# Optimization experiments

Hardware: AMD Instinct MI355X
Metric: run time of the kernel (lower is better)

## Reference

```python
import jax, jax.numpy as jnp
import numpy as np

N_POINTS = 65536
DIM = 8
E0 = N_POINTS - 1      # H0 generators (edges killing components)
E1 = 2_000_000         # H1 generators (birth edge + death edge)


def setup_inputs() -> dict:
    key = jax.random.key(0)
    k1, k2, k3 = jax.random.split(key, 3)
    points = jax.random.normal(k1, (N_POINTS, DIM), dtype=jnp.float32)
    verts0 = jax.random.randint(k2, (E0, 2), 0, N_POINTS, dtype=jnp.int64)
    verts1 = jax.random.randint(k3, (E1, 4), 0, N_POINTS, dtype=jnp.int64)
    return {"points": points, "verts0": verts0, "verts1": verts1}


def reference(points, verts0, verts1):
    # H0 death times: distance between the two vertices of each killing edge.
    # deaths[i] = || points[verts0[i,0]] - points[verts0[i,1]] ||
    d0 = points[verts0[:, 0]] - points[verts0[:, 1]]        # [E0, D]
    deaths = jnp.linalg.norm(d0, axis=-1)                    # [E0]

    # H1 diagram: birth = ||p[v0]-p[v1]||, death = ||p[v2]-p[v3]||,
    # computed as paired gathers on columns (0,2) vs (1,3) like the original.
    a = points[verts1[:, jnp.array([0, 2])]]                 # [E1, 2, D]
    b = points[verts1[:, jnp.array([1, 3])]]                 # [E1, 2, D]
    dgm1 = jnp.linalg.norm(a - b, axis=-1)                   # [E1, 2]
    return deaths, dgm1
```

## Files before the change

kernel.cpp:

```cpp
#include <hip/hip_runtime.h>
#include <hip/hip_fp16.h>
#include <math.h>


typedef int  v2i __attribute__((ext_vector_type(2)));

__global__ __launch_bounds__(256) void cvt_kernel(
    const float* __restrict__ pts, __half* __restrict__ out, int n4) {
    int i = blockIdx.x * blockDim.x + threadIdx.x;
    if (i < n4) {
        float4 f = ((const float4*)pts)[i];
        __half2 h0 = __floats2half2_rn(f.x, f.y);
        __half2 h1 = __floats2half2_rn(f.z, f.w);
        ((__half2*)out)[2 * i]     = h0;
        ((__half2*)out)[2 * i + 1] = h1;
    }
}

__device__ __forceinline__ float2 u2f2(unsigned u) {
    __half2 h = *reinterpret_cast<__half2*>(&u);
    return __half22float2(h);
}

__device__ __forceinline__ float dist8h(const uint4* __restrict__ p, int ia, int ib) {
    uint4 a = p[ia];
    uint4 b = p[ib];
    float2 ax = u2f2(a.x), ay = u2f2(a.y), az = u2f2(a.z), aw = u2f2(a.w);
    float2 bx = u2f2(b.x), by = u2f2(b.y), bz = u2f2(b.z), bw = u2f2(b.w);
    float d0 = ax.x - bx.x, d1 = ax.y - bx.y;
    float d2 = ay.x - by.x, d3 = ay.y - by.y;
    float d4 = az.x - bz.x, d5 = az.y - bz.y;
    float d6 = aw.x - bw.x, d7 = aw.y - bw.y;
    float s = d0 * d0 + d1 * d1 + d2 * d2 + d3 * d3
            + d4 * d4 + d5 * d5 + d6 * d6 + d7 * d7;
    return sqrtf(s);
}

__global__ __launch_bounds__(256) void rips_kernel_h2(
    const __half* __restrict__ points16,
    const int* __restrict__ verts0,
    const int* __restrict__ verts1,
    float* __restrict__ out,
    int e0, int e1) {
    int tid = blockIdx.x * blockDim.x + threadIdx.x;
    const uint4* p = (const uint4*)points16;
    int n1 = 2 * e1;
    if (tid < n1) {
        v2i v = __builtin_nontemporal_load((const v2i*)verts1 + tid);
        float r = dist8h(p, v.x, v.y);
        __builtin_nontemporal_store(r, out + e0 + tid);
    } else {
        int j = tid - n1;
        if (j < e0) {
            v2i v = __builtin_nontemporal_load((const v2i*)verts0 + j);
            float r = dist8h(p, v.x, v.y);
            __builtin_nontemporal_store(r, out + j);
        }
    }
}

__device__ __forceinline__ float dist8f(const float4* __restrict__ p, int ia, int ib) {
    float4 a0 = p[2 * ia], a1 = p[2 * ia + 1];
    float4 b0 = p[2 * ib], b1 = p[2 * ib + 1];
    float d0 = a0.x - b0.x, d1 = a0.y - b0.y, d2 = a0.z - b0.z, d3 = a0.w - b0.w;
    float d4 = a1.x - b1.x, d5 = a1.y - b1.y, d6 = a1.z - b1.z, d7 = a1.w - b1.w;
    return sqrtf(d0*d0 + d1*d1 + d2*d2 + d3*d3 + d4*d4 + d5*d5 + d6*d6 + d7*d7);
}

__global__ __launch_bounds__(256) void rips_kernel_f2(
    const float* __restrict__ points,
    const int* __restrict__ verts0,
    const int* __restrict__ verts1,
    float* __restrict__ out,
    int e0, int e1) {
    int tid = blockIdx.x * blockDim.x + threadIdx.x;
    const float4* p = (const float4*)points;
    int n1 = 2 * e1;
    if (tid < n1) {
        v2i v = __builtin_nontemporal_load((const v2i*)verts1 + tid);
        float r = dist8f(p, v.x, v.y);
        __builtin_nontemporal_store(r, out + e0 + tid);
    } else {
        int j = tid - n1;
        if (j < e0) {
            v2i v = __builtin_nontemporal_load((const v2i*)verts0 + j);
            float r = dist8f(p, v.x, v.y);
            __builtin_nontemporal_store(r, out + j);
        }
    }
}

extern "C" void kernel_launch(void* const* d_in, const int* in_sizes, int n_in,
                              void* d_out, int out_size, void* d_ws, size_t ws_size,
                              hipStream_t stream) {
    const float* points = (const float*)d_in[0];
    const int* verts0   = (const int*)d_in[1];
    const int* verts1   = (const int*)d_in[2];
    float* out = (float*)d_out;

    int npts_flat = in_sizes[0];
    int e0 = in_sizes[1] / 2;
    int e1 = in_sizes[2] / 4;

    int total = 2 * e1 + e0;
    int block = 256;
    int grid = (total + block - 1) / block;

    size_t fp16_bytes = (size_t)npts_flat * sizeof(__half);
    if (ws_size >= fp16_bytes) {
        __half* p16 = (__half*)d_ws;
        int n4 = npts_flat / 4;
        cvt_kernel<<<(n4 + 255) / 256, 256, 0, stream>>>(points, p16, n4);
        rips_kernel_h2<<<grid, block, 0, stream>>>(p16, verts0, verts1, out, e0, e1);
    } else {
        rips_kernel_f2<<<grid, block, 0, stream>>>(points, verts0, verts1, out, e0, e1);
    }
}
```

Baseline: 120.3 us.

## Process two H1 rows per thread and swizzle blocks across XCDs

Each thread now handles two H1 rows, issuing two 16-byte index loads, eight independent fp16 point gathers and four output stores. The H0 edges and an odd-row tail get a separate path. Block indices are remapped so that contiguous ranges of work land on the same XCD, which should improve L2 locality. The aim is more memory-level parallelism per thread and fewer threads, at the cost of higher register pressure and one quarter as many waves available to hide latency.

```diff
diff --git a/kernel.cpp b/kernel.cpp
--- a/kernel.cpp
+++ b/kernel.cpp
@@ -3,7 +3,8 @@
 #include <math.h>
 
 
-typedef int  v2i __attribute__((ext_vector_type(2)));
+typedef int v4i __attribute__((ext_vector_type(4)));
+typedef int v2i __attribute__((ext_vector_type(2)));
 
 __global__ __launch_bounds__(256) void cvt_kernel(
     const float* __restrict__ pts, __half* __restrict__ out, int n4) {
@@ -22,9 +23,7 @@
     return __half22float2(h);
 }
 
-__device__ __forceinline__ float dist8h(const uint4* __restrict__ p, int ia, int ib) {
-    uint4 a = p[ia];
-    uint4 b = p[ib];
+__device__ __forceinline__ float dist8v(uint4 a, uint4 b) {
     float2 ax = u2f2(a.x), ay = u2f2(a.y), az = u2f2(a.z), aw = u2f2(a.w);
     float2 bx = u2f2(b.x), by = u2f2(b.y), bz = u2f2(b.z), bw = u2f2(b.w);
     float d0 = ax.x - bx.x, d1 = ax.y - bx.y;
@@ -36,25 +35,62 @@
     return sqrtf(s);
 }
 
-__global__ __launch_bounds__(256) void rips_kernel_h2(
+__device__ __forceinline__ int xcd_swizzle(int b, int nwg) {
+    int q = nwg >> 3, r = nwg & 7;
+    int xcd = b & 7, off = b >> 3;
+    int base = (xcd < r) ? xcd * (q + 1) : r * (q + 1) + (xcd - r) * q;
+    return base + off;
+}
+
+__global__ __launch_bounds__(256) void rips_kernel_h8(
     const __half* __restrict__ points16,
     const int* __restrict__ verts0,
     const int* __restrict__ verts1,
     float* __restrict__ out,
     int e0, int e1) {
-    int tid = blockIdx.x * blockDim.x + threadIdx.x;
+    int sb = xcd_swizzle(blockIdx.x, gridDim.x);
+    int tid = sb * blockDim.x + threadIdx.x;
     const uint4* p = (const uint4*)points16;
-    int n1 = 2 * e1;
-    if (tid < n1) {
-        v2i v = __builtin_nontemporal_load((const v2i*)verts1 + tid);
-        float r = dist8h(p, v.x, v.y);
-        __builtin_nontemporal_store(r, out + e0 + tid);
+    int npair = e1 >> 1;
+    int rem   = e1 & 1;
+    if (tid < npair) {
+        const v4i* v1 = (const v4i*)verts1;
+        v4i va = __builtin_nontemporal_load(v1 + 2 * tid);
+        v4i vb = __builtin_nontemporal_load(v1 + 2 * tid + 1);
+        uint4 g0 = p[va.x];
+        uint4 g1 = p[va.y];
+        uint4 g2 = p[va.z];
+        uint4 g3 = p[va.w];
+        uint4 g4 = p[vb.x];
+        uint4 g5 = p[vb.y];
+        uint4 g6 = p[vb.z];
+        uint4 g7 = p[vb.w];
+        float r0 = dist8v(g0, g1);
+        float r1 = dist8v(g2, g3);
+        float r2 = dist8v(g4, g5);
+        float r3 = dist8v(g6, g7);
+        float* o = out + e0 + 4 * tid;
+        __builtin_nontemporal_store(r0, o);
+        __builtin_nontemporal_store(r1, o + 1);
+        __builtin_nontemporal_store(r2, o + 2);
+        __builtin_nontemporal_store(r3, o + 3);
     } else {
-        int j = tid - n1;
-        if (j < e0) {
-            v2i v = __builtin_nontemporal_load((const v2i*)verts0 + j);
-            float r = dist8h(p, v.x, v.y);
-            __builtin_nontemporal_store(r, out + j);
+        int j = tid - npair;
+        if (j < rem) {
+            int row = e1 - 1;
+            v2i v = __builtin_nontemporal_load((const v2i*)verts1 + 2 * row);
+            v2i w = __builtin_nontemporal_load((const v2i*)verts1 + 2 * row + 1);
+            float r0 = dist8v(p[v.x], p[v.y]);
+            float r1 = dist8v(p[w.x], p[w.y]);
+            __builtin_nontemporal_store(r0, out + e0 + 2 * row);
+            __builtin_nontemporal_store(r1, out + e0 + 2 * row + 1);
+        } else {
+            j -= rem;
+            if (j < e0) {
+                v2i v = __builtin_nontemporal_load((const v2i*)verts0 + j);
+                float r = dist8v(p[v.x], p[v.y]);
+                __builtin_nontemporal_store(r, out + j);
+            }
         }
     }
 }
@@ -102,17 +138,22 @@
     int e0 = in_sizes[1] / 2;
     int e1 = in_sizes[2] / 4;
 
-    int total = 2 * e1 + e0;
-    int block = 256;
-    int grid = (total + block - 1) / block;
-
     size_t fp16_bytes = (size_t)npts_flat * sizeof(__half);
     if (ws_size >= fp16_bytes) {
         __half* p16 = (__half*)d_ws;
         int n4 = npts_flat / 4;
         cvt_kernel<<<(n4 + 255) / 256, 256, 0, stream>>>(points, p16, n4);
-        rips_kernel_h2<<<grid, block, 0, stream>>>(p16, verts0, verts1, out, e0, e1);
+
+        int npair = e1 / 2;
+        int rem   = e1 & 1;
+        int total = npair + rem + e0;
+        int block = 256;
+        int grid = (total + block - 1) / block;
+        rips_kernel_h8<<<grid, block, 0, stream>>>(p16, verts0, verts1, out, e0, e1);
     } else {
+        int total = 2 * e1 + e0;
+        int block = 256;
+        int grid = (total + block - 1) / block;
         rips_kernel_f2<<<grid, block, 0, stream>>>(points, verts0, verts1, out, e0, e1);
     }
 }
```

After: 121.9 us. No clear change (+1.3%).

## Stage fp16 point table in output buffer and process full H1 rows per thread

Applied to the files above, without the earlier changes.

The fp16 copy of the points now goes into the start of the output buffer instead of the workspace. The main kernel computes every H1 row whose outputs lie past that table region, reading the fp16 table. A second head kernel then computes the overlapping rows and the H0 deaths from the fp32 points, which overwrites the table. Each H1 thread now loads all four vertex indices as one 16-byte load and writes two outputs, halving thread count. This removes the workspace dependency and reduces index-load instructions, at the cost of an extra launch and a serial dependency between kernels.

```diff
diff --git a/kernel.cpp b/kernel.cpp
--- a/kernel.cpp
+++ b/kernel.cpp
@@ -3,7 +3,8 @@
 #include <math.h>
 
 
-typedef int  v2i __attribute__((ext_vector_type(2)));
+typedef int v4i __attribute__((ext_vector_type(4)));
+typedef int v2i __attribute__((ext_vector_type(2)));
 
 __global__ __launch_bounds__(256) void cvt_kernel(
     const float* __restrict__ pts, __half* __restrict__ out, int n4) {
@@ -22,41 +23,14 @@
     return __half22float2(h);
 }
 
-__device__ __forceinline__ float dist8h(const uint4* __restrict__ p, int ia, int ib) {
-    uint4 a = p[ia];
-    uint4 b = p[ib];
+__device__ __forceinline__ float dist8v(uint4 a, uint4 b) {
     float2 ax = u2f2(a.x), ay = u2f2(a.y), az = u2f2(a.z), aw = u2f2(a.w);
     float2 bx = u2f2(b.x), by = u2f2(b.y), bz = u2f2(b.z), bw = u2f2(b.w);
     float d0 = ax.x - bx.x, d1 = ax.y - bx.y;
     float d2 = ay.x - by.x, d3 = ay.y - by.y;
     float d4 = az.x - bz.x, d5 = az.y - bz.y;
     float d6 = aw.x - bw.x, d7 = aw.y - bw.y;
-    float s = d0 * d0 + d1 * d1 + d2 * d2 + d3 * d3
-            + d4 * d4 + d5 * d5 + d6 * d6 + d7 * d7;
-    return sqrtf(s);
-}
-
-__global__ __launch_bounds__(256) void rips_kernel_h2(
-    const __half* __restrict__ points16,
-    const int* __restrict__ verts0,
-    const int* __restrict__ verts1,
-    float* __restrict__ out,
-    int e0, int e1) {
-    int tid = blockIdx.x * blockDim.x + threadIdx.x;
-    const uint4* p = (const uint4*)points16;
-    int n1 = 2 * e1;
-    if (tid < n1) {
-        v2i v = __builtin_nontemporal_load((const v2i*)verts1 + tid);
-        float r = dist8h(p, v.x, v.y);
-        __builtin_nontemporal_store(r, out + e0 + tid);
-    } else {
-        int j = tid - n1;
-        if (j < e0) {
-            v2i v = __builtin_nontemporal_load((const v2i*)verts0 + j);
-            float r = dist8h(p, v.x, v.y);
-            __builtin_nontemporal_store(r, out + j);
-        }
-    }
+    return sqrtf(d0*d0 + d1*d1 + d2*d2 + d3*d3 + d4*d4 + d5*d5 + d6*d6 + d7*d7);
 }
 
 __device__ __forceinline__ float dist8f(const float4* __restrict__ p, int ia, int ib) {
@@ -65,6 +39,46 @@
     float d0 = a0.x - b0.x, d1 = a0.y - b0.y, d2 = a0.z - b0.z, d3 = a0.w - b0.w;
     float d4 = a1.x - b1.x, d5 = a1.y - b1.y, d6 = a1.z - b1.z, d7 = a1.w - b1.w;
     return sqrtf(d0*d0 + d1*d1 + d2*d2 + d3*d3 + d4*d4 + d5*d5 + d6*d6 + d7*d7);
+}
+
+__global__ __launch_bounds__(256) void rips_main(
+    const __half* table,
+    const int* __restrict__ verts1,
+    float* out,
+    int e0, int r0, int e1) {
+    int t = blockIdx.x * blockDim.x + threadIdx.x;
+    int row = r0 + t;
+    if (row < e1) {
+        const uint4* p = (const uint4*)table;
+        v4i v = __builtin_nontemporal_load((const v4i*)verts1 + row);
+        float d0 = dist8v(p[v.x], p[v.y]);
+        float d1 = dist8v(p[v.z], p[v.w]);
+        __builtin_nontemporal_store(d0, out + e0 + 2 * row);
+        __builtin_nontemporal_store(d1, out + e0 + 2 * row + 1);
+    }
+}
+
+__global__ __launch_bounds__(256) void rips_head(
+    const float* __restrict__ points,
+    const int* __restrict__ verts0,
+    const int* __restrict__ verts1,
+    float* __restrict__ out,
+    int e0, int r0) {
+    int t = blockIdx.x * blockDim.x + threadIdx.x;
+    const float4* p = (const float4*)points;
+    if (t < r0) {
+        v4i v = __builtin_nontemporal_load((const v4i*)verts1 + t);
+        float d0 = dist8f(p, v.x, v.y);
+        float d1 = dist8f(p, v.z, v.w);
+        __builtin_nontemporal_store(d0, out + e0 + 2 * t);
+        __builtin_nontemporal_store(d1, out + e0 + 2 * t + 1);
+    } else {
+        int j = t - r0;
+        if (j < e0) {
+            v2i v = __builtin_nontemporal_load((const v2i*)verts0 + j);
+            __builtin_nontemporal_store(dist8f(p, v.x, v.y), out + j);
+        }
+    }
 }
 
 __global__ __launch_bounds__(256) void rips_kernel_f2(
@@ -78,14 +92,12 @@
     int n1 = 2 * e1;
     if (tid < n1) {
         v2i v = __builtin_nontemporal_load((const v2i*)verts1 + tid);
-        float r = dist8f(p, v.x, v.y);
-        __builtin_nontemporal_store(r, out + e0 + tid);
+        __builtin_nontemporal_store(dist8f(p, v.x, v.y), out + e0 + tid);
     } else {
         int j = tid - n1;
         if (j < e0) {
             v2i v = __builtin_nontemporal_load((const v2i*)verts0 + j);
-            float r = dist8f(p, v.x, v.y);
-            __builtin_nontemporal_store(r, out + j);
+            __builtin_nontemporal_store(dist8f(p, v.x, v.y), out + j);
         }
     }
 }
@@ -102,17 +114,39 @@
     int e0 = in_sizes[1] / 2;
     int e1 = in_sizes[2] / 4;
 
-    int total = 2 * e1 + e0;
     int block = 256;
-    int grid = (total + block - 1) / block;
 
-    size_t fp16_bytes = (size_t)npts_flat * sizeof(__half);
-    if (ws_size >= fp16_bytes) {
-        __half* p16 = (__half*)d_ws;
+    long long tableFloats = (long long)npts_flat / 2;
+    long long outFloats   = (long long)e0 + 2LL * e1;
+
+    long long r0ll = 0;
+    if (tableFloats > e0) r0ll = (tableFloats - e0 + 1) / 2;
+
+    bool ok = (npts_flat % 8 == 0) &&
+              (outFloats > tableFloats) &&
+              (r0ll <= (long long)e1);
+
+    if (ok) {
+        int r0 = (int)r0ll;
         int n4 = npts_flat / 4;
-        cvt_kernel<<<(n4 + 255) / 256, 256, 0, stream>>>(points, p16, n4);
-        rips_kernel_h2<<<grid, block, 0, stream>>>(p16, verts0, verts1, out, e0, e1);
+        cvt_kernel<<<(n4 + 255) / 256, 256, 0, stream>>>(
+            points, (__half*)out, n4);
+        int mainRows = e1 - r0;
+        if (mainRows > 0) {
+            int grid = (mainRows + block - 1) / block;
+            rips_main<<<grid, block, 0, stream>>>(
+                (const __half*)out, verts1, out, e0, r0, e1);
+        }
+        int headThreads = r0 + e0;
+        if (headThreads > 0) {
+            int grid = (headThreads + block - 1) / block;
+            rips_head<<<grid, block, 0, stream>>>(
+                points, verts0, verts1, out, e0, r0);
+        }
     } else {
-        rips_kernel_f2<<<grid, block, 0, stream>>>(points, verts0, verts1, out, e0, e1);
+        int total = 2 * e1 + e0;
+        int grid = (total + block - 1) / block;
+        rips_kernel_f2<<<grid, block, 0, stream>>>(
+            points, verts0, verts1, out, e0, e1);
     }
 }
```

Measured after the change: 126.5 us. +5.1%, slower.
